# Optimization experiments

Measured on AMD Instinct MI355X. Metric: run time of the kernel, lower is better.

Reference implementation:

```python
import jax, jax.numpy as jnp
import numpy as np

N_NODES = 100000
N_EDGES = 1600000
IN_DIM = 128
HIDDEN = 128
N_GRAPHS = 256


def setup_inputs() -> dict:
    key = jax.random.key(0)
    ks = jax.random.split(key, 12)
    x = jax.random.normal(ks[0], (N_NODES, IN_DIM), dtype=jnp.float32)
    edge_index = jax.random.randint(ks[1], (2, N_EDGES), 0, N_NODES, dtype=jnp.int64)
    batch = jnp.sort(jax.random.randint(ks[2], (N_NODES,), 0, N_GRAPHS, dtype=jnp.int64))
    s = 0.05
    W1 = jax.random.normal(ks[3], (IN_DIM, HIDDEN), dtype=jnp.float32) * s
    b1 = jnp.zeros((HIDDEN,), dtype=jnp.float32)
    W2 = jax.random.normal(ks[4], (HIDDEN, HIDDEN), dtype=jnp.float32) * s
    b2 = jnp.zeros((HIDDEN,), dtype=jnp.float32)
    W3 = jax.random.normal(ks[5], (HIDDEN, HIDDEN), dtype=jnp.float32) * s
    b3 = jnp.zeros((HIDDEN,), dtype=jnp.float32)
    Wh = jax.random.normal(ks[6], (HIDDEN, 2), dtype=jnp.float32) * s
    bh = jnp.zeros((2,), dtype=jnp.float32)
    return {"x": x, "edge_index": edge_index, "batch": batch,
            "W1": W1, "b1": b1, "W2": W2, "b2": b2, "W3": W3, "b3": b3,
            "Wh": Wh, "bh": bh}


def _gcn_structure(edge_index, n_nodes):
    # PyG GCNConv default: add self-loops, symmetric deg^-1/2 normalization.
    loop = jnp.arange(n_nodes, dtype=edge_index.dtype)
    src = jnp.concatenate([edge_index[0], loop])  # message source j
    dst = jnp.concatenate([edge_index[1], loop])  # aggregate at i
    deg = jax.ops.segment_sum(jnp.ones_like(dst, dtype=jnp.float32), dst,
                              num_segments=n_nodes)
    dinv = jnp.where(deg > 0, jax.lax.rsqrt(deg), 0.0)
    norm = dinv[src] * dinv[dst]  # [E + N]
    return src, dst, norm


def _gcn_conv(x, W, b, src, dst, norm, n_nodes):
    h = x @ W  # dense transform first (PyG order)
    msg = h[src] * norm[:, None]  # gather + per-edge scale
    agg = jax.ops.segment_sum(msg, dst, num_segments=n_nodes)  # scatter-add
    return agg + b


def reference(x, edge_index, batch, W1, b1, W2, b2, W3, b3, Wh, bh):
    n = x.shape[0]
    src, dst, norm = _gcn_structure(edge_index, n)
    # dropout is a no-op in eval mode (training=False)
    h = jax.nn.relu(_gcn_conv(x, W1, b1, src, dst, norm, n))
    h = jax.nn.relu(_gcn_conv(h, W2, b2, src, dst, norm, n))
    h = jax.nn.relu(_gcn_conv(h, W3, b3, src, dst, norm, n))
    # global_mean_pool over graph ids
    sums = jax.ops.segment_sum(h, batch, num_segments=N_GRAPHS)
    cnts = jax.ops.segment_sum(jnp.ones((n,), dtype=h.dtype), batch,
                               num_segments=N_GRAPHS)
    pooled = sums / jnp.maximum(cnts, 1.0)[:, None]
    return pooled @ Wh + bh  # [N_GRAPHS, 2]
```

## Files before the change

kernel.cpp:

```cpp
#include <hip/hip_runtime.h>


#define D 128
#define NB_SHIFT 8
#define BCAP 8192
#define EPB 4096

typedef unsigned int uint;
typedef unsigned short ushort;
typedef __attribute__((ext_vector_type(8))) short short8;
typedef __attribute__((ext_vector_type(4))) float f32x4;

__device__ __forceinline__ ushort f2bf(float f) {
    uint u = __float_as_uint(f);
    uint r = (u + 0x7fffu + ((u >> 16) & 1u)) >> 16;
    return (ushort)r;
}
__device__ __forceinline__ float bf2f(ushort b) {
    return __uint_as_float(((uint)b) << 16);
}
__device__ __forceinline__ float q15f(uint q) {
    return __uint_as_float(0x30000000u | (q << 13));
}

__device__ __forceinline__ void async_cp16(const ushort* g, ushort* lds_uniform) {
    __builtin_amdgcn_global_load_lds(
        (const __attribute__((address_space(1))) unsigned int*)g,
        (__attribute__((address_space(3))) unsigned int*)lds_uniform,
        16, 0, 0);
}

__device__ __forceinline__ void bucketA_body(const int* __restrict__ src,
                                             const int* __restrict__ dst, int E,
                                             int nbk, int* __restrict__ gcur,
                                             uint* __restrict__ arena, int bid,
                                             int* hist, int* rbase) {
    int t = threadIdx.x;
    int e0 = bid * EPB;
    int e1 = min(e0 + EPB, E);
    for (int i = t; i < nbk; i += 256) hist[i] = 0;
    __syncthreads();
    for (int e = e0 + t; e < e1; e += 256)
        atomicAdd(&hist[dst[e] >> NB_SHIFT], 1);
    __syncthreads();
    for (int i = t; i < nbk; i += 256) {
        int c = hist[i];
        rbase[i] = (c > 0) ? atomicAdd(&gcur[i], c) : 0;
        hist[i] = 0;
    }
    __syncthreads();
    for (int e = e0 + t; e < e1; e += 256) {
        int d = dst[e];
        int s = src[e];
        int b = d >> NB_SHIFT;
        int pos = rbase[b] + atomicAdd(&hist[b], 1);
        if (pos < BCAP)
            arena[(size_t)b * BCAP + pos] =
                ((uint)(d & ((1 << NB_SHIFT) - 1)) << 17) | (uint)s;
    }
}

template <bool AF32>
__device__ __forceinline__ void gemm_body(const void* __restrict__ Ain,
                                          const ushort* __restrict__ Wf,
                                          ushort* __restrict__ out, int N,
                                          int rowb, ushort* As) {
    int t = threadIdx.x;

    if (AF32) {
        const float* A = (const float*)Ain;
#pragma unroll
        for (int i = 0; i < 8; i++) {
            int u = i * 256 + t;
            int row = u >> 5, c4 = u & 31;
            int grow = rowb + row;
            float4 v = make_float4(0.f, 0.f, 0.f, 0.f);
            if (grow < N) v = *(const float4*)(A + (size_t)grow * D + c4 * 4);
            uint2 p;
            p.x = (uint)f2bf(v.x) | ((uint)f2bf(v.y) << 16);
            p.y = (uint)f2bf(v.z) | ((uint)f2bf(v.w) << 16);
            int byteoff = row * 256 + ((c4 * 8) ^ ((row & 7) << 4));
            *(uint2*)((char*)As + byteoff) = p;
        }
    } else {
        const ushort* A = (const ushort*)Ain;
#pragma unroll
        for (int i = 0; i < 4; i++) {
            int u = i * 256 + t;
            int row = u >> 4, cp = u & 15;
            int grow = rowb + row;
            if (grow >= N) grow = N - 1;
            int gc = cp ^ (row & 7);
            const ushort* gp = A + (size_t)grow * D + gc * 8;
            ushort* lb = As + (size_t)(i * 256 + (t & 192)) * 8;
            async_cp16(gp, lb);
        }
        asm volatile("s_waitcnt vmcnt(0)" ::: "memory");
    }
    __syncthreads();

    int wave = t >> 6, lane = t & 63;
    const short8* Wf8 = (const short8*)Wf;

    short8 bhi[2][4], blo[2][4];
#pragma unroll
    for (int j = 0; j < 2; j++) {
        int nt = wave * 2 + j;
#pragma unroll
        for (int kt = 0; kt < 4; kt++) {
            bhi[j][kt] = Wf8[(size_t)((0 * 4 + kt) * 8 + nt) * 64 + lane];
            blo[j][kt] = Wf8[(size_t)((1 * 4 + kt) * 8 + nt) * 64 + lane];
        }
    }

    f32x4 acc[4][2];
#pragma unroll
    for (int m = 0; m < 4; m++)
#pragma unroll
        for (int j = 0; j < 2; j++) acc[m][j] = (f32x4){0.f, 0.f, 0.f, 0.f};

#pragma unroll
    for (int m = 0; m < 4; m++) {
        int r = m * 16 + (lane & 15);
#pragma unroll
        for (int kt = 0; kt < 4; kt++) {
            int raw = kt * 64 + (lane >> 4) * 16;
            short8 a = *(const short8*)((const char*)As + r * 256 + (raw ^ ((r & 7) << 4)));
#pragma unroll
            for (int j = 0; j < 2; j++) {
                acc[m][j] = __builtin_amdgcn_mfma_f32_16x16x32_bf16(a, bhi[j][kt], acc[m][j], 0, 0, 0);
                acc[m][j] = __builtin_amdgcn_mfma_f32_16x16x32_bf16(a, blo[j][kt], acc[m][j], 0, 0, 0);
            }
        }
    }

#pragma unroll
    for (int m = 0; m < 4; m++) {
#pragma unroll
        for (int j = 0; j < 2; j++) {
            int colb = (wave * 2 + j) * 16 + (lane & 15);
#pragma unroll
            for (int jj = 0; jj < 4; jj++) {
                int grow = rowb + m * 16 + (lane >> 4) * 4 + jj;
                if (grow < N)
                    out[(size_t)grow * D + colb] = f2bf(acc[m][j][jj]);
            }
        }
    }
}

__global__ __launch_bounds__(256) void k_build_gemm1(const int* __restrict__ src,
                                                     const int* __restrict__ dst, int E,
                                                     int nbk, int* __restrict__ gcur,
                                                     uint* __restrict__ arena, int nA,
                                                     const float* __restrict__ x,
                                                     const ushort* __restrict__ Wf,
                                                     ushort* __restrict__ T, int N) {
    __shared__ ushort As[64 * D];
    if ((int)blockIdx.x < nA) {
        int* hist = (int*)As;
        int* rbase = hist + 512;
        bucketA_body(src, dst, E, nbk, gcur, arena, blockIdx.x, hist, rbase);
    } else {
        gemm_body<true>(x, Wf, T, N, (blockIdx.x - nA) * 64, As);
    }
}

template <bool AF32>
__global__ __launch_bounds__(256) void k_gemm(const void* __restrict__ Ain,
                                              const ushort* __restrict__ Wf,
                                              ushort* __restrict__ out, int N) {
    __shared__ ushort As[64 * D];
    gemm_body<AF32>(Ain, Wf, out, N, blockIdx.x * 64, As);
}

__global__ __launch_bounds__(256) void k_degB3(const uint* __restrict__ arena,
                                               const int* __restrict__ gcur,
                                               int nbk, int N, int E,
                                               float* __restrict__ dinv,
                                               int* __restrict__ row_start) {
    int b = blockIdx.x;
    int t = threadIdx.x;
    __shared__ int hist[256];
    __shared__ int sc[256];
    __shared__ int red[256];
    hist[t] = 0;
    __syncthreads();
    int cnt = min(gcur[b], BCAP);
    const uint* seg = arena + (size_t)b * BCAP;
    for (int i = t; i < cnt; i += 256)
        atomicAdd(&hist[seg[i] >> 17], 1);

    int p = 0;
    if (t < b) p += gcur[t];
    if (t + 256 < b) p += gcur[t + 256];
    red[t] = p;
    __syncthreads();
    for (int off2 = 128; off2 > 0; off2 >>= 1) {
        if (t < off2) red[t] += red[t + off2];
        __syncthreads();
    }
    int bbase = red[0];

    int c = hist[t];
    sc[t] = c;
    __syncthreads();
    for (int off2 = 1; off2 < 256; off2 <<= 1) {
        int x = (t >= off2) ? sc[t - off2] : 0;
        __syncthreads();
        sc[t] += x;
        __syncthreads();
    }
    int node = (b << NB_SHIFT) + t;
    if (node < N) {
        dinv[node] = rsqrtf((float)(c + 1));
        row_start[node] = bbase + sc[t] - c;
    }
    if (b == 0 && t == 0) row_start[N] = E;
}

__global__ __launch_bounds__(256) void k_bucketB(const uint* __restrict__ arena,
                                                 const int* __restrict__ gcur,
                                                 const int* __restrict__ row_start,
                                                 const float* __restrict__ dinv,
                                                 int N, uint* __restrict__ csr) {
    int b = blockIdx.x;
    int t = threadIdx.x;
    int n0 = b << NB_SHIFT;
    int nn = min(1 << NB_SHIFT, N - n0);
    __shared__ float sdinv[256];
    __shared__ int sstart[256];
    __shared__ int scur[256];
    __shared__ uint sout[BCAP];
    for (int i = t; i < nn; i += 256) {
        sdinv[i]  = dinv[n0 + i];
        sstart[i] = row_start[n0 + i];
        scur[i]   = 0;
    }
    __syncthreads();
    int cnt = min(gcur[b], BCAP);
    int csr0 = sstart[0];
    for (int i = t; i < cnt; i += 256) {
        uint en = arena[(size_t)b * BCAP + i];
        int dl = en >> 17;
        int s  = en & 0x1FFFF;
        float nrm = dinv[s] * sdinv[dl];
        uint q = ((__float_as_uint(nrm) + 0x1000u) >> 13) & 0x7FFFu;
        int pos = atomicAdd(&scur[dl], 1);
        sout[(sstart[dl] - csr0) + pos] = ((uint)s << 15) | q;
    }
    __syncthreads();
    for (int i = t; i < cnt; i += 256)
        csr[csr0 + i] = sout[i];
}

__global__ void k_wsplit3(const float* __restrict__ W1, const float* __restrict__ W2,
                          const float* __restrict__ W3, ushort* __restrict__ Wf,
                          int* __restrict__ gcur, int nbk) {
    int gidx = blockIdx.x * blockDim.x + threadIdx.x;
    if (gidx < nbk) gcur[gidx] = 0;
    if (gidx >= 3 * 32768) return;
    int which = gidx >> 15;
    int idx = gidx & 32767;
    const float* W = (which == 0) ? W1 : (which == 1) ? W2 : W3;
    int i  = idx & 7;
    int l  = (idx >> 3) & 63;
    int nt = (idx >> 9) & 7;
    int kt = (idx >> 12) & 3;
    int h  = idx >> 14;
    int k = kt * 32 + (l >> 4) * 8 + i;
    int n = nt * 16 + (l & 15);
    float w = W[k * D + n];
    ushort hi = f2bf(w);
    ushort v = (h == 0) ? hi : f2bf(w - bf2f(hi));
    Wf[gidx] = v;
}

__device__ __forceinline__ void agg_core(const ushort* __restrict__ T,
                                         const uint* __restrict__ csr,
                                         int beg, int end, int col,
                                         float& a0, float& a1) {
    if (beg >= end) return;
    int lane16 = threadIdx.x & 15;
    uint cur = csr[min(beg + lane16, end - 1)];
    for (int e = beg; e < end; e += 16) {
        uint nxt = 0;
        int en = e + 16;
        if (en < end) nxt = csr[min(en + lane16, end - 1)];
        uint v[16];
        float nn[16];
#pragma unroll
        for (int q = 0; q < 16; q++) {
            uint c = __builtin_amdgcn_readlane(cur, q);
            nn[q] = (e + q < end) ? q15f(c & 0x7FFFu) : 0.f;
            v[q] = *(const uint*)(T + (size_t)(c >> 15) * D + col);
        }
#pragma unroll
        for (int q = 0; q < 16; q++) {
            a0 = fmaf(nn[q], __uint_as_float(v[q] << 16), a0);
            a1 = fmaf(nn[q], __uint_as_float(v[q] & 0xffff0000u), a1);
        }
        cur = nxt;
    }
}

__global__ __launch_bounds__(256) void k_agg(const ushort* __restrict__ T,
                                             const float* __restrict__ dinv,
                                             const int* __restrict__ row_start,
                                             const uint* __restrict__ csr,
                                             const float* __restrict__ bias,
                                             ushort* __restrict__ out, int N) {
    int node = __builtin_amdgcn_readfirstlane(blockIdx.x * 4 + (threadIdx.x >> 6));
    if (node >= N) return;
    int lane = threadIdx.x & 63;
    int col = lane * 2;

    float di = dinv[node];
    uint vs = *(const uint*)(T + (size_t)node * D + col);
    float sw = di * di;
    float a0 = sw * __uint_as_float(vs << 16);
    float a1 = sw * __uint_as_float(vs & 0xffff0000u);

    agg_core(T, csr, row_start[node], row_start[node + 1], col, a0, a1);

    a0 = fmaxf(a0 + bias[col], 0.f);
    a1 = fmaxf(a1 + bias[col + 1], 0.f);
    ushort2 o; o.x = f2bf(a0); o.y = f2bf(a1);
    *(ushort2*)(out + (size_t)node * D + col) = o;
}

__global__ __launch_bounds__(256) void k_agg_head(const ushort* __restrict__ T,
                                                  const float* __restrict__ dinv,
                                                  const int* __restrict__ row_start,
                                                  const uint* __restrict__ csr,
                                                  const float* __restrict__ bias,
                                                  const float* __restrict__ Wh,
                                                  float2* __restrict__ y, int N) {
    int node = __builtin_amdgcn_readfirstlane(blockIdx.x * 4 + (threadIdx.x >> 6));
    if (node >= N) return;
    int lane = threadIdx.x & 63;
    int col = lane * 2;

    float di = dinv[node];
    uint vs = *(const uint*)(T + (size_t)node * D + col);
    float sw = di * di;
    float a0 = sw * __uint_as_float(vs << 16);
    float a1 = sw * __uint_as_float(vs & 0xffff0000u);

    agg_core(T, csr, row_start[node], row_start[node + 1], col, a0, a1);

    a0 = fmaxf(a0 + bias[col], 0.f);
    a1 = fmaxf(a1 + bias[col + 1], 0.f);

    float p0 = a0 * Wh[col * 2 + 0] + a1 * Wh[(col + 1) * 2 + 0];
    float p1 = a0 * Wh[col * 2 + 1] + a1 * Wh[(col + 1) * 2 + 1];
#pragma unroll
    for (int off = 32; off > 0; off >>= 1) {
        p0 += __shfl_xor(p0, off);
        p1 += __shfl_xor(p1, off);
    }
    if (lane == 0) y[node] = make_float2(p0, p1);
}

__global__ __launch_bounds__(256) void k_pool2(const float2* __restrict__ y,
                                               const int* __restrict__ batch, int N,
                                               const float* __restrict__ bh,
                                               float* __restrict__ out) {
    int g = blockIdx.x;
    int t = threadIdx.x;
    int lo = 0, hi = N;
    while (lo < hi) { int m = (lo + hi) >> 1; if (batch[m] < g) lo = m + 1; else hi = m; }
    int beg = lo;
    lo = 0; hi = N;
    while (lo < hi) { int m = (lo + hi) >> 1; if (batch[m] < g + 1) lo = m + 1; else hi = m; }
    int endi = lo;

    float s0 = 0.f, s1 = 0.f;
    for (int i = beg + t; i < endi; i += 256) {
        float2 v = y[i];
        s0 += v.x; s1 += v.y;
    }
    __shared__ float r0[256], r1[256];
    r0[t] = s0; r1[t] = s1;
    __syncthreads();
    for (int off = 128; off > 0; off >>= 1) {
        if (t < off) { r0[t] += r0[t + off]; r1[t] += r1[t + off]; }
        __syncthreads();
    }
    if (t == 0) {
        float cnt = (float)((endi - beg) > 0 ? (endi - beg) : 1);
        out[g * 2 + 0] = r0[0] / cnt + bh[0];
        out[g * 2 + 1] = r1[0] / cnt + bh[1];
    }
}

extern "C" void kernel_launch(void* const* d_in, const int* in_sizes, int n_in,
                              void* d_out, int out_size, void* d_ws, size_t ws_size,
                              hipStream_t stream) {
    const float* x   = (const float*)d_in[0];
    const int* eidx  = (const int*)d_in[1];
    const int* batch = (const int*)d_in[2];
    const float* W1 = (const float*)d_in[3];
    const float* b1 = (const float*)d_in[4];
    const float* W2 = (const float*)d_in[5];
    const float* b2 = (const float*)d_in[6];
    const float* W3 = (const float*)d_in[7];
    const float* b3 = (const float*)d_in[8];
    const float* Wh = (const float*)d_in[9];
    const float* bh = (const float*)d_in[10];

    int E = in_sizes[1] / 2;
    int N = in_sizes[2];
    int ngraphs = out_size / 2;
    const int* src = eidx;
    const int* dst = eidx + E;
    int nbk = (N + (1 << NB_SHIFT) - 1) >> NB_SHIFT;

    char* ws = (char*)d_ws;
    size_t off = 0;
    auto alloc = [&](size_t bytes) -> void* {
        void* p = ws + off;
        off = (off + bytes + 255) & ~(size_t)255;
        return p;
    };
    ushort* Hbf      = (ushort*)alloc((size_t)N * D * 2);
    ushort* T        = (ushort*)alloc((size_t)N * D * 2);
    ushort* Wf       = (ushort*)alloc(3 * 32768 * 2);
    float*  dinv     = (float*)alloc((size_t)N * 4);
    int*    row_start= (int*)alloc((size_t)(N + 1) * 4);
    int*    gcur     = (int*)alloc((size_t)nbk * 4);
    float2* y        = (float2*)alloc((size_t)N * 8);
    uint*   csr      = (uint*)alloc((size_t)E * 4);
    uint*   arena    = (uint*)alloc((size_t)nbk * BCAP * 4);
    (void)ws_size;

    k_wsplit3<<<384, 256, 0, stream>>>(W1, W2, W3, Wf, gcur, nbk);

    int gemm_grid = (N + 63) / 64;
    int agg_grid = (N + 3) / 4;
    int nA = (E + EPB - 1) / EPB;

    k_build_gemm1<<<nA + gemm_grid, 256, 0, stream>>>(src, dst, E, nbk, gcur, arena,
                                                      nA, x, Wf, T, N);
    k_degB3<<<nbk, 256, 0, stream>>>(arena, gcur, nbk, N, E, dinv, row_start);
    k_bucketB<<<nbk, 256, 0, stream>>>(arena, gcur, row_start, dinv, N, csr);

    k_agg<<<agg_grid, 256, 0, stream>>>(T, dinv, row_start, csr, b1, Hbf, N);
    k_gemm<false><<<gemm_grid, 256, 0, stream>>>(Hbf, Wf + 32768, T, N);
    k_agg<<<agg_grid, 256, 0, stream>>>(T, dinv, row_start, csr, b2, Hbf, N);
    k_gemm<false><<<gemm_grid, 256, 0, stream>>>(Hbf, Wf + 65536, T, N);
    k_agg_head<<<agg_grid, 256, 0, stream>>>(T, dinv, row_start, csr, b3, Wh, y, N);
    k_pool2<<<ngraphs, 256, 0, stream>>>(y, batch, N, bh, (float*)d_out);
}
```

Before: 282.6 us.

## Overlap aggregation tail with next-layer GEMM head and stage bucket writes in LDS

```diff
diff --git a/kernel.cpp b/kernel.cpp
--- a/kernel.cpp
+++ b/kernel.cpp
@@ -5,6 +5,7 @@
 #define NB_SHIFT 8
 #define BCAP 8192
 #define EPB 4096
+#define N2SPLIT 65536
 
 typedef unsigned int uint;
 typedef unsigned short ushort;
@@ -34,33 +35,57 @@
                                              const int* __restrict__ dst, int E,
                                              int nbk, int* __restrict__ gcur,
                                              uint* __restrict__ arena, int bid,
-                                             int* hist, int* rbase) {
+                                             uint* smem) {
+    uint* image  = smem;
+    int*  cnt    = (int*)(smem + 4096);
+    int*  excl   = (int*)(smem + 4608);
+    int*  rb     = (int*)(smem + 5120);
+    int*  cursor = (int*)(smem + 5632);
     int t = threadIdx.x;
     int e0 = bid * EPB;
     int e1 = min(e0 + EPB, E);
-    for (int i = t; i < nbk; i += 256) hist[i] = 0;
+
+    for (int i = t; i < 512; i += 256) { cnt[i] = 0; cursor[i] = 0; }
     __syncthreads();
     for (int e = e0 + t; e < e1; e += 256)
-        atomicAdd(&hist[dst[e] >> NB_SHIFT], 1);
+        atomicAdd(&cnt[dst[e] >> NB_SHIFT], 1);
     __syncthreads();
     for (int i = t; i < nbk; i += 256) {
-        int c = hist[i];
-        rbase[i] = (c > 0) ? atomicAdd(&gcur[i], c) : 0;
-        hist[i] = 0;
-    }
-    __syncthreads();
+        int c = cnt[i];
+        rb[i] = (c > 0) ? atomicAdd(&gcur[i], c) : 0;
+    }
+    excl[t] = cnt[t];
+    excl[t + 256] = cnt[t + 256];
+    __syncthreads();
+    for (int off = 1; off < 512; off <<= 1) {
+        int v0 = (t >= off) ? excl[t - off] : 0;
+        int v1 = (t + 256 >= off) ? excl[t + 256 - off] : 0;
+        __syncthreads();
+        excl[t] += v0;
+        excl[t + 256] += v1;
+        __syncthreads();
+    }
     for (int e = e0 + t; e < e1; e += 256) {
         int d = dst[e];
         int s = src[e];
         int b = d >> NB_SHIFT;
-        int pos = rbase[b] + atomicAdd(&hist[b], 1);
-        if (pos < BCAP)
-            arena[(size_t)b * BCAP + pos] =
-                ((uint)(d & ((1 << NB_SHIFT) - 1)) << 17) | (uint)s;
-    }
-}
-
-template <bool AF32>
+        int pos = atomicAdd(&cursor[b], 1);
+        image[(excl[b] - cnt[b]) + pos] =
+            ((uint)(d & ((1 << NB_SHIFT) - 1)) << 17) | (uint)s;
+    }
+    __syncthreads();
+    int wave = t >> 6, lane = t & 63;
+    for (int b = wave; b < nbk; b += 4) {
+        int c = cnt[b];
+        int lbase = excl[b] - c;
+        int g = rb[b];
+        for (int i = lane; i < c; i += 64)
+            if (g + i < BCAP)
+                arena[(size_t)b * BCAP + g + i] = image[lbase + i];
+    }
+}
+
+template <bool AF32, bool PRELOAD>
 __device__ __forceinline__ void gemm_body(const void* __restrict__ Ain,
                                           const ushort* __restrict__ Wf,
                                           ushort* __restrict__ out, int N,
@@ -102,34 +127,53 @@
     int wave = t >> 6, lane = t & 63;
     const short8* Wf8 = (const short8*)Wf;
 
-    short8 bhi[2][4], blo[2][4];
-#pragma unroll
-    for (int j = 0; j < 2; j++) {
-        int nt = wave * 2 + j;
-#pragma unroll
-        for (int kt = 0; kt < 4; kt++) {
-            bhi[j][kt] = Wf8[(size_t)((0 * 4 + kt) * 8 + nt) * 64 + lane];
-            blo[j][kt] = Wf8[(size_t)((1 * 4 + kt) * 8 + nt) * 64 + lane];
-        }
-    }
-
     f32x4 acc[4][2];
 #pragma unroll
     for (int m = 0; m < 4; m++)
 #pragma unroll
         for (int j = 0; j < 2; j++) acc[m][j] = (f32x4){0.f, 0.f, 0.f, 0.f};
 
-#pragma unroll
-    for (int m = 0; m < 4; m++) {
-        int r = m * 16 + (lane & 15);
-#pragma unroll
-        for (int kt = 0; kt < 4; kt++) {
-            int raw = kt * 64 + (lane >> 4) * 16;
-            short8 a = *(const short8*)((const char*)As + r * 256 + (raw ^ ((r & 7) << 4)));
-#pragma unroll
-            for (int j = 0; j < 2; j++) {
-                acc[m][j] = __builtin_amdgcn_mfma_f32_16x16x32_bf16(a, bhi[j][kt], acc[m][j], 0, 0, 0);
-                acc[m][j] = __builtin_amdgcn_mfma_f32_16x16x32_bf16(a, blo[j][kt], acc[m][j], 0, 0, 0);
+    if (PRELOAD) {
+        short8 bhi[2][4], blo[2][4];
+#pragma unroll
+        for (int j = 0; j < 2; j++) {
+            int nt = wave * 2 + j;
+#pragma unroll
+            for (int kt = 0; kt < 4; kt++) {
+                bhi[j][kt] = Wf8[(size_t)((0 * 4 + kt) * 8 + nt) * 64 + lane];
+                blo[j][kt] = Wf8[(size_t)((1 * 4 + kt) * 8 + nt) * 64 + lane];
+            }
+        }
+#pragma unroll
+        for (int m = 0; m < 4; m++) {
+            int r = m * 16 + (lane & 15);
+#pragma unroll
+            for (int kt = 0; kt < 4; kt++) {
+                int raw = kt * 64 + (lane >> 4) * 16;
+                short8 a = *(const short8*)((const char*)As + r * 256 + (raw ^ ((r & 7) << 4)));
+#pragma unroll
+                for (int j = 0; j < 2; j++) {
+                    acc[m][j] = __builtin_amdgcn_mfma_f32_16x16x32_bf16(a, bhi[j][kt], acc[m][j], 0, 0, 0);
+                    acc[m][j] = __builtin_amdgcn_mfma_f32_16x16x32_bf16(a, blo[j][kt], acc[m][j], 0, 0, 0);
+                }
+            }
+        }
+    } else {
+#pragma unroll
+        for (int m = 0; m < 4; m++) {
+            int r = m * 16 + (lane & 15);
+#pragma unroll
+            for (int kt = 0; kt < 4; kt++) {
+                int raw = kt * 64 + (lane >> 4) * 16;
+                short8 a = *(const short8*)((const char*)As + r * 256 + (raw ^ ((r & 7) << 4)));
+#pragma unroll
+                for (int j = 0; j < 2; j++) {
+                    int nt = wave * 2 + j;
+                    short8 bh = Wf8[(size_t)((0 * 4 + kt) * 8 + nt) * 64 + lane];
+                    short8 bl = Wf8[(size_t)((1 * 4 + kt) * 8 + nt) * 64 + lane];
+                    acc[m][j] = __builtin_amdgcn_mfma_f32_16x16x32_bf16(a, bh, acc[m][j], 0, 0, 0);
+                    acc[m][j] = __builtin_amdgcn_mfma_f32_16x16x32_bf16(a, bl, acc[m][j], 0, 0, 0);
+                }
             }
         }
     }
@@ -156,22 +200,19 @@
                                                      const float* __restrict__ x,
                                                      const ushort* __restrict__ Wf,
                                                      ushort* __restrict__ T, int N) {
-    __shared__ ushort As[64 * D];
+    __shared__ uint smem[6144];
     if ((int)blockIdx.x < nA) {
-        int* hist = (int*)As;
-        int* rbase = hist + 512;
-        bucketA_body(src, dst, E, nbk, gcur, arena, blockIdx.x, hist, rbase);
+        bucketA_body(src, dst, E, nbk, gcur, arena, blockIdx.x, smem);
     } else {
-        gemm_body<true>(x, Wf, T, N, (blockIdx.x - nA) * 64, As);
-    }
-}
-
-template <bool AF32>
+        gemm_body<true, true>(x, Wf, T, N, (blockIdx.x - nA) * 64, (ushort*)smem);
+    }
+}
+
 __global__ __launch_bounds__(256) void k_gemm(const void* __restrict__ Ain,
                                               const ushort* __restrict__ Wf,
-                                              ushort* __restrict__ out, int N) {
+                                              ushort* __restrict__ out, int N, int base) {
     __shared__ ushort As[64 * D];
-    gemm_body<AF32>(Ain, Wf, out, N, blockIdx.x * 64, As);
+    gemm_body<false, true>(Ain, Wf, out, N, base + blockIdx.x * 64, As);
 }
 
 __global__ __launch_bounds__(256) void k_degB3(const uint* __restrict__ arena,
@@ -304,29 +345,56 @@
     }
 }
 
+__device__ __forceinline__ void agg_node(const ushort* __restrict__ T,
+                                         const float* __restrict__ dinv,
+                                         const int* __restrict__ row_start,
+                                         const uint* __restrict__ csr,
+                                         const float* __restrict__ bias,
+                                         ushort* __restrict__ out, int node) {
+    int lane = threadIdx.x & 63;
+    int col = lane * 2;
+    float di = dinv[node];
+    uint vs = *(const uint*)(T + (size_t)node * D + col);
+    float sw = di * di;
+    float a0 = sw * __uint_as_float(vs << 16);
+    float a1 = sw * __uint_as_float(vs & 0xffff0000u);
+    agg_core(T, csr, row_start[node], row_start[node + 1], col, a0, a1);
+    a0 = fmaxf(a0 + bias[col], 0.f);
+    a1 = fmaxf(a1 + bias[col + 1], 0.f);
+    ushort2 o; o.x = f2bf(a0); o.y = f2bf(a1);
+    *(ushort2*)(out + (size_t)node * D + col) = o;
+}
+
 __global__ __launch_bounds__(256) void k_agg(const ushort* __restrict__ T,
                                              const float* __restrict__ dinv,
                                              const int* __restrict__ row_start,
                                              const uint* __restrict__ csr,
                                              const float* __restrict__ bias,
-                                             ushort* __restrict__ out, int N) {
-    int node = __builtin_amdgcn_readfirstlane(blockIdx.x * 4 + (threadIdx.x >> 6));
-    if (node >= N) return;
-    int lane = threadIdx.x & 63;
-    int col = lane * 2;
-
-    float di = dinv[node];
-    uint vs = *(const uint*)(T + (size_t)node * D + col);
-    float sw = di * di;
-    float a0 = sw * __uint_as_float(vs << 16);
-    float a1 = sw * __uint_as_float(vs & 0xffff0000u);
-
-    agg_core(T, csr, row_start[node], row_start[node + 1], col, a0, a1);
-
-    a0 = fmaxf(a0 + bias[col], 0.f);
-    a1 = fmaxf(a1 + bias[col + 1], 0.f);
-    ushort2 o; o.x = f2bf(a0); o.y = f2bf(a1);
-    *(ushort2*)(out + (size_t)node * D + col) = o;
+                                             ushort* __restrict__ out,
+                                             int base, int limit) {
+    int node = __builtin_amdgcn_readfirstlane(base + blockIdx.x * 4 + (threadIdx.x >> 6));
+    if (node >= limit) return;
+    agg_node(T, dinv, row_start, csr, bias, out, node);
+}
+
+__global__ __launch_bounds__(256, 6) void k_aggmix(const ushort* __restrict__ T,
+                                                   const float* __restrict__ dinv,
+                                                   const int* __restrict__ row_start,
+                                                   const uint* __restrict__ csr,
+                                                   const float* __restrict__ bias,
+                                                   ushort* __restrict__ Hout,
+                                                   int aggBase, int limit, int nAggBlk,
+                                                   const ushort* __restrict__ Ain,
+                                                   const ushort* __restrict__ Wf,
+                                                   ushort* __restrict__ Tout, int N) {
+    __shared__ ushort As[64 * D];
+    if ((int)blockIdx.x < nAggBlk) {
+        int node = __builtin_amdgcn_readfirstlane(aggBase + blockIdx.x * 4 + (threadIdx.x >> 6));
+        if (node >= limit) return;
+        agg_node(T, dinv, row_start, csr, bias, Hout, node);
+    } else {
+        gemm_body<false, false>(Ain, Wf, Tout, N, (blockIdx.x - nAggBlk) * 64, As);
+    }
 }
 
 __global__ __launch_bounds__(256) void k_agg_head(const ushort* __restrict__ T,
@@ -415,6 +483,7 @@
     const int* src = eidx;
     const int* dst = eidx + E;
     int nbk = (N + (1 << NB_SHIFT) - 1) >> NB_SHIFT;
+    int N2 = (N2SPLIT < N) ? N2SPLIT : (N / 128) * 64;
 
     char* ws = (char*)d_ws;
     size_t off = 0;
@@ -424,7 +493,8 @@
         return p;
     };
     ushort* Hbf      = (ushort*)alloc((size_t)N * D * 2);
-    ushort* T        = (ushort*)alloc((size_t)N * D * 2);
+    ushort* Ta       = (ushort*)alloc((size_t)N * D * 2);
+    ushort* Tb       = (ushort*)alloc((size_t)N * D * 2);
     ushort* Wf       = (ushort*)alloc(3 * 32768 * 2);
     float*  dinv     = (float*)alloc((size_t)N * 4);
     int*    row_start= (int*)alloc((size_t)(N + 1) * 4);
@@ -437,18 +507,30 @@
     k_wsplit3<<<384, 256, 0, stream>>>(W1, W2, W3, Wf, gcur, nbk);
 
     int gemm_grid = (N + 63) / 64;
+    int nA = (E + EPB - 1) / EPB;
+    int aggA_grid = N2 / 4;
+    int aggB_grid = (N - N2 + 3) / 4;
+    int gemmA_grid = N2 / 64;
+    int gemmB_grid = (N - N2 + 63) / 64;
     int agg_grid = (N + 3) / 4;
-    int nA = (E + EPB - 1) / EPB;
 
     k_build_gemm1<<<nA + gemm_grid, 256, 0, stream>>>(src, dst, E, nbk, gcur, arena,
-                                                      nA, x, Wf, T, N);
+                                                      nA, x, Wf, Ta, N);
     k_degB3<<<nbk, 256, 0, stream>>>(arena, gcur, nbk, N, E, dinv, row_start);
     k_bucketB<<<nbk, 256, 0, stream>>>(arena, gcur, row_start, dinv, N, csr);
 
-    k_agg<<<agg_grid, 256, 0, stream>>>(T, dinv, row_start, csr, b1, Hbf, N);
-    k_gemm<false><<<gemm_grid, 256, 0, stream>>>(Hbf, Wf + 32768, T, N);
-    k_agg<<<agg_grid, 256, 0, stream>>>(T, dinv, row_start, csr, b2, Hbf, N);
-    k_gemm<false><<<gemm_grid, 256, 0, stream>>>(Hbf, Wf + 65536, T, N);
-    k_agg_head<<<agg_grid, 256, 0, stream>>>(T, dinv, row_start, csr, b3, Wh, y, N);
+    k_agg<<<aggA_grid, 256, 0, stream>>>(Ta, dinv, row_start, csr, b1, Hbf, 0, N2);
+    k_aggmix<<<aggB_grid + gemmA_grid, 256, 0, stream>>>(Ta, dinv, row_start, csr, b1,
+                                                         Hbf, N2, N, aggB_grid,
+                                                         Hbf, Wf + 32768, Tb, N);
+    k_gemm<<<gemmB_grid, 256, 0, stream>>>(Hbf, Wf + 32768, Tb, N, N2);
+
+    k_agg<<<aggA_grid, 256, 0, stream>>>(Tb, dinv, row_start, csr, b2, Hbf, 0, N2);
+    k_aggmix<<<aggB_grid + gemmA_grid, 256, 0, stream>>>(Tb, dinv, row_start, csr, b2,
+                                                         Hbf, N2, N, aggB_grid,
+                                                         Hbf, Wf + 65536, Ta, N);
+    k_gemm<<<gemmB_grid, 256, 0, stream>>>(Hbf, Wf + 65536, Ta, N, N2);
+
+    k_agg_head<<<agg_grid, 256, 0, stream>>>(Ta, dinv, row_start, csr, b3, Wh, y, N);
     k_pool2<<<ngraphs, 256, 0, stream>>>(y, batch, N, bh, (float*)d_out);
 }
```

After: 301.4 us. 1.07x slower.
